# Kernel tuning notes

Hardware: AMD Instinct MI355X
Metric: run time of the kernel (lower is better)

Reference implementation:

```python
import jax, jax.numpy as jnp
import numpy as np

ALPHA = 0.2          # LeakyReLU negative slope
NEG_INF = -9e15      # mask value used by the original module

def setup_inputs() -> dict:
    key = jax.random.key(0)
    k1, k2, k3, k4 = jax.random.split(key, 4)
    B, N, F_in, F_out = 8, 2048, 128, 64
    h = jax.random.normal(k1, (B, N, F_in), dtype=jnp.float32)
    # dense 0/1 adjacency with self-loops so every softmax row is valid
    adj = jax.random.randint(k2, (B, N, N), 0, 2).astype(jnp.float32)
    adj = jnp.maximum(adj, jnp.eye(N, dtype=jnp.float32)[None])
    # xavier_uniform with gain=1.414 (as in torch init)
    gain = 1.414
    limW = gain * np.sqrt(6.0 / (F_in + F_out))
    W = jax.random.uniform(k3, (F_in, F_out), jnp.float32, -limW, limW)
    lima = gain * np.sqrt(6.0 / (2 * F_out + 1))
    attention_w = jax.random.uniform(k4, (2 * F_out, 1), jnp.float32, -lima, lima)
    return {"h": h, "adj": adj, "W": W, "attention_w": attention_w}

def reference(h, adj, W, attention_w):
    # hidden: (B, N, F_out)
    hidden = jnp.matmul(h, W)
    F_out = W.shape[1]
    # Decompose additive attention: e[b,i,j] = leakyrelu(Wh_i . a1 + Wh_j . a2)
    # (mathematically identical to the concat + matmul in the original, but
    # avoids materializing the (B,N,N,2F) tensor)
    a1 = attention_w[:F_out, 0]   # (F_out,)
    a2 = attention_w[F_out:, 0]   # (F_out,)
    s1 = jnp.einsum('bnf,f->bn', hidden, a1)  # (B, N)
    s2 = jnp.einsum('bnf,f->bn', hidden, a2)  # (B, N)
    e = s1[:, :, None] + s2[:, None, :]       # (B, N, N)
    e = jnp.where(e >= 0, e, ALPHA * e)       # LeakyReLU
    scores = jnp.where(adj > 0, e * adj, NEG_INF)
    attention = jax.nn.softmax(scores, axis=2)
    # dropout is identity at inference (training=False)
    h_prime = jnp.matmul(attention, hidden)   # (B, N, F_out)
    return jax.nn.elu(h_prime)                # concat=True -> ELU
```

## Files before the change

kernel.cpp:

```cpp
#include <hip/hip_runtime.h>
#include <stdint.h>

typedef float f32x2 __attribute__((ext_vector_type(2)));
typedef float f32x4 __attribute__((ext_vector_type(4)));
typedef uint32_t u32x4 __attribute__((ext_vector_type(4)));
typedef short s16x8 __attribute__((ext_vector_type(8)));

#define BB   8
#define NN   2048
#define FIN  128
#define FOUT 64

__device__ __forceinline__ uint32_t cvt_pk_bf16(float lo, float hi) {
  uint32_t r;
  asm("v_cvt_pk_bf16_f32 %0, %1, %2" : "=v"(r) : "v"(lo), "v"(hi));
  return r;
}

__device__ __forceinline__ s16x8 mk_s16x8(uint32_t a, uint32_t b, uint32_t c, uint32_t d) {
  union { uint32_t u[4]; s16x8 v; } x;
  x.u[0] = a; x.u[1] = b; x.u[2] = c; x.u[3] = d;
  return x.v;
}

__global__ void k1_hidden(const float* __restrict__ h, const float* __restrict__ W,
                          const float* __restrict__ attw, ushort* __restrict__ hidT,
                          float* __restrict__ s1, float* __restrict__ s2) {
  __shared__ ushort wlds[FOUT * 136];
  const int tid = threadIdx.x;

  for (int idx = tid; idx < FIN * FOUT; idx += 256) {
    int k = idx >> 6, c = idx & 63;
    wlds[c * 136 + k] = (ushort)(cvt_pk_bf16(W[idx], 0.f) & 0xffffu);
  }
  __syncthreads();

  const int bid = ((blockIdx.x & 7) << 5) | (blockIdx.x >> 3);
  const int lane = tid & 63, wid = tid >> 6;
  const int q = lane & 15, g = lane >> 4;
  const int wrow0 = bid * 64 + wid * 16;
  const int b  = wrow0 >> 11;
  const int n0 = wrow0 & (NN - 1);

  const float* hrow = h + (size_t)(wrow0 + q) * FIN + 8 * g;

  f32x4 acc[4];
  #pragma unroll
  for (int nt = 0; nt < 4; ++nt) acc[nt] = {0.f, 0.f, 0.f, 0.f};

  #pragma unroll
  for (int kk = 0; kk < 4; ++kk) {
    f32x4 h0 = *(const f32x4*)(hrow + 32 * kk);
    f32x4 h1 = *(const f32x4*)(hrow + 32 * kk + 4);
    s16x8 A = mk_s16x8(cvt_pk_bf16(h0[0], h0[1]), cvt_pk_bf16(h0[2], h0[3]),
                       cvt_pk_bf16(h1[0], h1[1]), cvt_pk_bf16(h1[2], h1[3]));
    #pragma unroll
    for (int nt = 0; nt < 4; ++nt) {
      s16x8 Bf = *(const s16x8*)(&wlds[(nt * 16 + q) * 136 + 32 * kk + 8 * g]);
      acc[nt] = __builtin_amdgcn_mfma_f32_16x16x32_bf16(A, Bf, acc[nt], 0, 0, 0);
    }
  }

  float a1v[4], a2v[4];
  #pragma unroll
  for (int nt = 0; nt < 4; ++nt) {
    a1v[nt] = attw[nt * 16 + q];
    a2v[nt] = attw[64 + nt * 16 + q];
  }
  float p1[4], p2[4];
  #pragma unroll
  for (int r = 0; r < 4; ++r) {
    float v1 = 0.f, v2 = 0.f;
    #pragma unroll
    for (int nt = 0; nt < 4; ++nt) { v1 += acc[nt][r] * a1v[nt]; v2 += acc[nt][r] * a2v[nt]; }
    #pragma unroll
    for (int m = 1; m < 16; m <<= 1) { v1 += __shfl_xor(v1, m, 64); v2 += __shfl_xor(v2, m, 64); }
    p1[r] = v1; p2[r] = v2;
  }
  if (q < 4) {
    int gr = wrow0 + 4 * g + q;
    float v1 = (q == 0) ? p1[0] : (q == 1) ? p1[1] : (q == 2) ? p1[2] : p1[3];
    float v2 = (q == 0) ? p2[0] : (q == 1) ? p2[1] : (q == 2) ? p2[2] : p2[3];
    s1[gr] = v1; s2[gr] = v2;
  }

  #pragma unroll
  for (int nt = 0; nt < 4; ++nt) {
    uint32_t lo = cvt_pk_bf16(acc[nt][0], acc[nt][1]);
    uint32_t hi = cvt_pk_bf16(acc[nt][2], acc[nt][3]);
    *(uint2*)(hidT + ((size_t)b * FOUT + nt * 16 + q) * NN + n0 + 4 * g) = make_uint2(lo, hi);
  }
}

__global__ __launch_bounds__(512, 4) void kF(
    const float* __restrict__ adj, const ushort* __restrict__ hidT,
    const float* __restrict__ s1g, const float* __restrict__ s2g,
    float* __restrict__ out) {
  __shared__ __align__(16) char smem[74240];
  float* s2l   = (float*)(smem + 65536);
  float* partl = (float*)(smem + 73728);

  const int tid = threadIdx.x;
  const int sb = ((blockIdx.x & 7) << 6) | (blockIdx.x >> 3);
  const int b  = sb >> 6;
  const int i0 = (sb & 63) << 5;

  const int lane = tid & 63, wid = tid >> 6;
  const int q = lane & 15, g = lane >> 4;
  const int rg = wid >> 2, jw = wid & 3;

  *(f32x4*)(s2l + tid * 4) = *(const f32x4*)(s2g + b * NN + tid * 4);
  const float s1r = s1g[b * NN + i0 + rg * 16 + q];

  const float* adjB = adj + ((size_t)(b * NN + i0 + wid)) * NN + lane * 2;
  const int f0 = tid >> 4, sl = tid & 15;
  const ushort* hBp = hidT + ((size_t)(b * FOUT + f0)) * NN + sl * 8;

  f32x2 a0, a1, a2, a3; u32x4 h0v, h1v;

#define LOADC(cc) do {                                                        \
    const float* p_ = adjB + (cc) * 128;                                      \
    a0 = *(const f32x2*)(p_);                                                 \
    a1 = *(const f32x2*)(p_ + (size_t) 8 * NN);                               \
    a2 = *(const f32x2*)(p_ + (size_t)16 * NN);                               \
    a3 = *(const f32x2*)(p_ + (size_t)24 * NN);                               \
    const ushort* q_ = hBp + (cc) * 128;                                      \
    h0v = *(const u32x4*)(q_);                                                \
    h1v = *(const u32x4*)(q_ + (size_t)32 * NN);                              \
  } while (0)

#define DSWC(B_) do {                                                         \
    char* db = smem + (B_) * 32768;                                           \
    const int aw = lane * 8;                                                  \
    *(f32x2*)(db + (wid     ) * 512 + (aw ^ (((wid     ) & 7) << 4))) = a0;   \
    *(f32x2*)(db + (wid +  8) * 512 + (aw ^ (((wid +  8) & 7) << 4))) = a1;   \
    *(f32x2*)(db + (wid + 16) * 512 + (aw ^ (((wid + 16) & 7) << 4))) = a2;   \
    *(f32x2*)(db + (wid + 24) * 512 + (aw ^ (((wid + 24) & 7) << 4))) = a3;   \
    char* d_ = db + 16384;                                                    \
    const int hw = (sl << 4) ^ ((f0 & 7) << 4);                               \
    *(u32x4*)(d_ + (f0     ) * 256 + hw) = h0v;                               \
    *(u32x4*)(d_ + (f0 + 32) * 256 + hw) = h1v;                               \
  } while (0)

  LOADC(0);
  DSWC(0);
  __syncthreads();

  f32x4 acc0 = {0,0,0,0}, acc1 = {0,0,0,0}, acc2 = {0,0,0,0}, acc3 = {0,0,0,0};
  float lsum = 0.f;
  const int xr = (q & 7) << 4;
  const int arow = rg * 16 + q;

  #pragma unroll
  for (int c = 0; c < 16; ++c) {
    if (c < 15) LOADC(c + 1);

    {
      const char* tb = smem + (c & 1) * 32768;
      const char* hL = tb + 16384;
      const int jb = jw * 128 + g * 32;
      f32x4 av0 = *(const f32x4*)(tb + arow * 512 + ((jb     ) ^ xr));
      f32x4 av1 = *(const f32x4*)(tb + arow * 512 + ((jb + 16) ^ xr));
      const int jl = jw * 32 + 8 * g;
      f32x4 t0 = *(const f32x4*)(s2l + c * 128 + jl);
      f32x4 t1 = *(const f32x4*)(s2l + c * 128 + jl + 4);
      const int hb_ = (jw * 64 + g * 16) ^ xr;
      u32x4 b0 = *(const u32x4*)(hL + (( 0 + q) << 8) + hb_);
      u32x4 b1 = *(const u32x4*)(hL + ((16 + q) << 8) + hb_);
      u32x4 b2 = *(const u32x4*)(hL + ((32 + q) << 8) + hb_);
      u32x4 b3 = *(const u32x4*)(hL + ((48 + q) << 8) + hb_);

      float e0 = s1r + t0[0], e1 = s1r + t0[1], e2 = s1r + t0[2], e3 = s1r + t0[3];
      float e4 = s1r + t1[0], e5 = s1r + t1[1], e6 = s1r + t1[2], e7 = s1r + t1[3];
      float p0 = av0[0] * __expf(fmaxf(e0, 0.2f * e0));
      float p1 = av0[1] * __expf(fmaxf(e1, 0.2f * e1));
      float p2 = av0[2] * __expf(fmaxf(e2, 0.2f * e2));
      float p3 = av0[3] * __expf(fmaxf(e3, 0.2f * e3));
      float p4 = av1[0] * __expf(fmaxf(e4, 0.2f * e4));
      float p5 = av1[1] * __expf(fmaxf(e5, 0.2f * e5));
      float p6 = av1[2] * __expf(fmaxf(e6, 0.2f * e6));
      float p7 = av1[3] * __expf(fmaxf(e7, 0.2f * e7));
      lsum += ((p0 + p1) + (p2 + p3)) + ((p4 + p5) + (p6 + p7));

      s16x8 A = mk_s16x8(cvt_pk_bf16(p0, p1), cvt_pk_bf16(p2, p3),
                         cvt_pk_bf16(p4, p5), cvt_pk_bf16(p6, p7));
      union { u32x4 u; s16x8 v; } w0, w1, w2, w3;
      w0.u = b0; w1.u = b1; w2.u = b2; w3.u = b3;
      acc0 = __builtin_amdgcn_mfma_f32_16x16x32_bf16(A, w0.v, acc0, 0, 0, 0);
      acc1 = __builtin_amdgcn_mfma_f32_16x16x32_bf16(A, w1.v, acc1, 0, 0, 0);
      acc2 = __builtin_amdgcn_mfma_f32_16x16x32_bf16(A, w2.v, acc2, 0, 0, 0);
      acc3 = __builtin_amdgcn_mfma_f32_16x16x32_bf16(A, w3.v, acc3, 0, 0, 0);
    }

    if (c < 15) DSWC((c + 1) & 1);
    __syncthreads();
  }

  lsum += __shfl_xor(lsum, 16, 64);
  lsum += __shfl_xor(lsum, 32, 64);
  if (lane < 16) partl[jw * 32 + rg * 16 + lane] = lsum;

  float* part = (float*)smem;
  #pragma unroll
  for (int r = 0; r < 4; ++r) {
    const int il = rg * 16 + 4 * g + r;
    part[(jw * 32 + il) * 64 +  0 + q] = acc0[r];
    part[(jw * 32 + il) * 64 + 16 + q] = acc1[r];
    part[(jw * 32 + il) * 64 + 32 + q] = acc2[r];
    part[(jw * 32 + il) * 64 + 48 + q] = acc3[r];
  }
  __syncthreads();

  #pragma unroll
  for (int k = 0; k < 4; ++k) {
    const int idx = tid + 512 * k;
    const int row = idx >> 6, col = idx & 63;
    float v  = (part[(0 * 32 + row) * 64 + col] + part[(1 * 32 + row) * 64 + col]) +
               (part[(2 * 32 + row) * 64 + col] + part[(3 * 32 + row) * 64 + col]);
    float li = (partl[0 * 32 + row] + partl[1 * 32 + row]) +
               (partl[2 * 32 + row] + partl[3 * 32 + row]);
    float hp = v / li;
    out[(size_t)(b * NN + i0 + row) * 64 + col] = (hp > 0.f) ? hp : expm1f(hp);
  }
}

extern "C" void kernel_launch(void* const* d_in, const int* in_sizes, int n_in,
                              void* d_out, int out_size, void* d_ws, size_t ws_size,
                              hipStream_t stream) {
  const float* h    = (const float*)d_in[0];
  const float* adj  = (const float*)d_in[1];
  const float* W    = (const float*)d_in[2];
  const float* attw = (const float*)d_in[3];
  float* out = (float*)d_out;

  char* ws = (char*)d_ws;
  ushort* hidT = (ushort*)ws;
  float*  s1   = (float*)(ws + (2u << 20));
  float*  s2   = (float*)(ws + (2u << 20) + (64u << 10));

  hipLaunchKernelGGL(k1_hidden, dim3(256), dim3(256), 0, stream, h, W, attw, hidT, s1, s2);
  hipLaunchKernelGGL(kF, dim3(512), dim3(512), 0, stream, adj, hidT, s1, s2, out);
}
```

Measured before the change: 40.16 us.

## Pre-swizzle hidden into MFMA fragment layout and load B operands from global

The first kernel now writes the bf16 hidden features already arranged in the per-lane MFMA B-fragment order. The attention kernel then loads B fragments straight from global/L2 instead of staging them through LDS. This halves the LDS footprint, which allows more resident blocks, and removes the LDS writes and reads for hidden. In exchange, each MFMA step issues global loads in the inner loop that are not prefetched a stage ahead, so latency may be exposed, and every wave re-reads the same fragments from cache.

```diff
diff --git a/kernel.cpp b/kernel.cpp
--- a/kernel.cpp
+++ b/kernel.cpp
@@ -24,7 +24,7 @@
 }
 
 __global__ void k1_hidden(const float* __restrict__ h, const float* __restrict__ W,
-                          const float* __restrict__ attw, ushort* __restrict__ hidT,
+                          const float* __restrict__ attw, ushort* __restrict__ hidF,
                           float* __restrict__ s1, float* __restrict__ s2) {
   __shared__ ushort wlds[FOUT * 136];
   const int tid = threadIdx.x;
@@ -84,21 +84,27 @@
     s1[gr] = v1; s2[gr] = v2;
   }
 
-  #pragma unroll
-  for (int nt = 0; nt < 4; ++nt) {
-    uint32_t lo = cvt_pk_bf16(acc[nt][0], acc[nt][1]);
-    uint32_t hi = cvt_pk_bf16(acc[nt][2], acc[nt][3]);
-    *(uint2*)(hidT + ((size_t)b * FOUT + nt * 16 + q) * NN + n0 + 4 * g) = make_uint2(lo, hi);
+  {
+    const int sj = n0 >> 5;
+    const int jo = (n0 & 31) + 4 * g;
+    const int g2 = jo >> 3, half = (jo >> 2) & 1;
+    #pragma unroll
+    for (int nt = 0; nt < 4; ++nt) {
+      uint32_t lo = cvt_pk_bf16(acc[nt][0], acc[nt][1]);
+      uint32_t hi = cvt_pk_bf16(acc[nt][2], acc[nt][3]);
+      ushort* dst = hidF + (((size_t)(b * 64 + sj) * 4 + nt) * 64 + g2 * 16 + q) * 8 + half * 4;
+      *(uint2*)dst = make_uint2(lo, hi);
+    }
   }
 }
 
 __global__ __launch_bounds__(512, 4) void kF(
-    const float* __restrict__ adj, const ushort* __restrict__ hidT,
+    const float* __restrict__ adj, const ushort* __restrict__ hidF,
     const float* __restrict__ s1g, const float* __restrict__ s2g,
     float* __restrict__ out) {
-  __shared__ __align__(16) char smem[74240];
-  float* s2l   = (float*)(smem + 65536);
-  float* partl = (float*)(smem + 73728);
+  __shared__ __align__(16) char smem[41472];
+  float* s2l   = (float*)(smem + 32768);
+  float* partl = (float*)(smem + 40960);
 
   const int tid = threadIdx.x;
   const int sb = ((blockIdx.x & 7) << 6) | (blockIdx.x >> 3);
@@ -113,10 +119,9 @@
   const float s1r = s1g[b * NN + i0 + rg * 16 + q];
 
   const float* adjB = adj + ((size_t)(b * NN + i0 + wid)) * NN + lane * 2;
-  const int f0 = tid >> 4, sl = tid & 15;
-  const ushort* hBp = hidT + ((size_t)(b * FOUT + f0)) * NN + sl * 8;
-
-  f32x2 a0, a1, a2, a3; u32x4 h0v, h1v;
+  const ushort* fragB = hidF + (size_t)(b * 64) * 2048 + lane * 8;
+
+  f32x2 a0, a1, a2, a3;
 
 #define LOADC(cc) do {                                                        \
     const float* p_ = adjB + (cc) * 128;                                      \
@@ -124,22 +129,15 @@
     a1 = *(const f32x2*)(p_ + (size_t) 8 * NN);                               \
     a2 = *(const f32x2*)(p_ + (size_t)16 * NN);                               \
     a3 = *(const f32x2*)(p_ + (size_t)24 * NN);                               \
-    const ushort* q_ = hBp + (cc) * 128;                                      \
-    h0v = *(const u32x4*)(q_);                                                \
-    h1v = *(const u32x4*)(q_ + (size_t)32 * NN);                              \
   } while (0)
 
 #define DSWC(B_) do {                                                         \
-    char* db = smem + (B_) * 32768;                                           \
+    char* db = smem + (B_) * 16384;                                           \
     const int aw = lane * 8;                                                  \
     *(f32x2*)(db + (wid     ) * 512 + (aw ^ (((wid     ) & 7) << 4))) = a0;   \
     *(f32x2*)(db + (wid +  8) * 512 + (aw ^ (((wid +  8) & 7) << 4))) = a1;   \
     *(f32x2*)(db + (wid + 16) * 512 + (aw ^ (((wid + 16) & 7) << 4))) = a2;   \
     *(f32x2*)(db + (wid + 24) * 512 + (aw ^ (((wid + 24) & 7) << 4))) = a3;   \
-    char* d_ = db + 16384;                                                    \
-    const int hw = (sl << 4) ^ ((f0 & 7) << 4);                               \
-    *(u32x4*)(d_ + (f0     ) * 256 + hw) = h0v;                               \
-    *(u32x4*)(d_ + (f0 + 32) * 256 + hw) = h1v;                               \
   } while (0)
 
   LOADC(0);
@@ -156,19 +154,19 @@
     if (c < 15) LOADC(c + 1);
 
     {
-      const char* tb = smem + (c & 1) * 32768;
-      const char* hL = tb + 16384;
+      const ushort* fb = fragB + (size_t)(c * 4 + jw) * 2048;
+      u32x4 b0 = *(const u32x4*)(fb);
+      u32x4 b1 = *(const u32x4*)(fb + 512);
+      u32x4 b2 = *(const u32x4*)(fb + 1024);
+      u32x4 b3 = *(const u32x4*)(fb + 1536);
+
+      const char* tb = smem + (c & 1) * 16384;
       const int jb = jw * 128 + g * 32;
       f32x4 av0 = *(const f32x4*)(tb + arow * 512 + ((jb     ) ^ xr));
       f32x4 av1 = *(const f32x4*)(tb + arow * 512 + ((jb + 16) ^ xr));
       const int jl = jw * 32 + 8 * g;
       f32x4 t0 = *(const f32x4*)(s2l + c * 128 + jl);
       f32x4 t1 = *(const f32x4*)(s2l + c * 128 + jl + 4);
-      const int hb_ = (jw * 64 + g * 16) ^ xr;
-      u32x4 b0 = *(const u32x4*)(hL + (( 0 + q) << 8) + hb_);
-      u32x4 b1 = *(const u32x4*)(hL + ((16 + q) << 8) + hb_);
-      u32x4 b2 = *(const u32x4*)(hL + ((32 + q) << 8) + hb_);
-      u32x4 b3 = *(const u32x4*)(hL + ((48 + q) << 8) + hb_);
 
       float e0 = s1r + t0[0], e1 = s1r + t0[1], e2 = s1r + t0[2], e3 = s1r + t0[3];
       float e4 = s1r + t1[0], e5 = s1r + t1[1], e6 = s1r + t1[2], e7 = s1r + t1[3];
@@ -234,10 +232,10 @@
   float* out = (float*)d_out;
 
   char* ws = (char*)d_ws;
-  ushort* hidT = (ushort*)ws;
+  ushort* hidF = (ushort*)ws;
   float*  s1   = (float*)(ws + (2u << 20));
   float*  s2   = (float*)(ws + (2u << 20) + (64u << 10));
 
-  hipLaunchKernelGGL(k1_hidden, dim3(256), dim3(256), 0, stream, h, W, attw, hidT, s1, s2);
-  hipLaunchKernelGGL(kF, dim3(512), dim3(512), 0, stream, adj, hidT, s1, s2, out);
-}
+  hipLaunchKernelGGL(k1_hidden, dim3(256), dim3(256), 0, stream, h, W, attw, hidF, s1, s2);
+  hipLaunchKernelGGL(kF, dim3(512), dim3(512), 0, stream, adj, hidF, s1, s2, out);
+}
```

Result: no change. 40.91 us (+1.9%).
